# Kernel optimization log

Hardware: AMD Instinct MI355X
Metric: run time of the kernel (lower is better)

Reference implementation:

```python
import jax, jax.numpy as jnp
import numpy as np

NUM_HEADS = 16
THETA = 10000.0


def setup_inputs() -> dict:
    key = jax.random.key(0)
    k1, k2, k3, k4 = jax.random.split(key, 4)
    B, T, D = 2, 2048, 1024
    x = jax.random.normal(k1, (B, T, D), dtype=jnp.float32)
    token_positions = jnp.sort(
        jax.random.randint(k2, (B, T), 0, 2048), axis=-1
    ).astype(jnp.int32)
    sigma_qkv = float(np.sqrt(2.0 / (D + 3 * D)))
    sigma_out = float(np.sqrt(2.0 / (D + D)))
    W_qkv = jax.random.normal(k3, (3 * D, D), dtype=jnp.float32) * sigma_qkv
    W_out = jax.random.normal(k4, (D, D), dtype=jnp.float32) * sigma_out
    return {"x": x, "token_positions": token_positions, "W_qkv": W_qkv, "W_out": W_out}


def _apply_rope(t, cos, sin):
    # t: [B, H, T, d_k]; cos/sin: [B, T, d_k//2]
    B, H, T, dk = t.shape
    t2 = t.reshape(B, H, T, dk // 2, 2)
    te, to = t2[..., 0], t2[..., 1]
    c = cos[:, None]  # [B, 1, T, dk//2]
    s = sin[:, None]
    ye = te * c - to * s
    yo = to * c + te * s
    return jnp.stack([ye, yo], axis=-1).reshape(B, H, T, dk)


def reference(x, token_positions, W_qkv, W_out):
    B, T, D = x.shape
    H = NUM_HEADS
    dk = D // H

    # fused QKV projection: [B, T, 3D] -> split (three, h, d) on last dim
    qkv = jnp.einsum("btd,od->bto", x, W_qkv).reshape(B, T, 3, H, dk)
    qkv = jnp.transpose(qkv, (2, 0, 3, 1, 4))  # [3, B, H, T, dk]
    q, k, v = qkv[0], qkv[1], qkv[2]

    # RoPE angles from token positions
    n = jnp.arange(dk // 2, dtype=jnp.float32)
    inv_freq = THETA ** (-2.0 * n / dk)  # [dk//2]
    angles = token_positions.astype(jnp.float32)[..., None] * inv_freq  # [B, T, dk//2]
    cos, sin = jnp.cos(angles), jnp.sin(angles)
    q = _apply_rope(q, cos, sin)
    k = _apply_rope(k, cos, sin)

    # causal scaled dot-product attention
    scores = jnp.einsum("bhid,bhjd->bhij", q, k) / jnp.sqrt(jnp.float32(dk))
    causal = jnp.tril(jnp.ones((T, T), dtype=bool))
    scores = jnp.where(causal, scores, -jnp.inf)
    probs = jax.nn.softmax(scores, axis=-1)
    attn = jnp.einsum("bhij,bhjd->bhid", probs, v)  # [B, H, T, dk]

    concat = jnp.transpose(attn, (0, 2, 1, 3)).reshape(B, T, D)
    return jnp.einsum("btd,od->bto", concat, W_out)
```

## Files before the change

### kernel.cpp

```cpp
#include <hip/hip_runtime.h>
#include <hip/hip_bf16.h>
#include <cmath>

#define T_SEQ 2048
#define D_MODEL 1024
#define NHEAD 16
#define DK 64

typedef short bf16x8 __attribute__((ext_vector_type(8)));
typedef float f32x4 __attribute__((ext_vector_type(4)));
typedef float f32x16 __attribute__((ext_vector_type(16)));
typedef unsigned uint2v __attribute__((ext_vector_type(2)));

union U8 { unsigned u[4]; bf16x8 v; };

#define VMCNT(n) asm volatile("s_waitcnt vmcnt(" #n ")" ::: "memory")
#define BAR() __builtin_amdgcn_s_barrier()
#define SFENCE() __builtin_amdgcn_sched_barrier(0)

__device__ __forceinline__ short f2b(float f) {
    unsigned u = __builtin_bit_cast(unsigned, f);
    unsigned r = (u + 0x7FFFu + ((u >> 16) & 1u)) >> 16;
    return (short)r;
}

__device__ __forceinline__ void gll16(const void* g, void* l) {
    __builtin_amdgcn_global_load_lds(
        (__attribute__((address_space(1))) void*)g,
        (__attribute__((address_space(3))) void*)l, 16, 0, 0);
}

__device__ __forceinline__ bf16x8 lds_frag(const short* base, int row, int chunk) {
    return *reinterpret_cast<const bf16x8*>(
        (const char*)base + row * 128 + ((chunk * 16) ^ ((row & 7) << 4)));
}

__device__ __forceinline__ unsigned pkbf16(float a, float b) {
    unsigned r;
    asm("v_cvt_pk_bf16_f32 %0, %1, %2" : "=v"(r) : "v"(a), "v"(b));
    return r;
}
__device__ __forceinline__ void pl32swap(unsigned& a, unsigned& b) {
    uint2v r = __builtin_amdgcn_permlane32_swap(a, b, false, false);
    a = r.x; b = r.y;
}

__global__ __launch_bounds__(256) void cvt_all(const float* __restrict__ x,
                                               const float* __restrict__ wq,
                                               const float* __restrict__ wo,
                                               const int* __restrict__ pos,
                                               short* __restrict__ xb,
                                               short* __restrict__ wqb,
                                               short* __restrict__ wob,
                                               float* __restrict__ ct,
                                               float* __restrict__ st) {
    int i = blockIdx.x * 256 + threadIdx.x;
    if (i >= 1048576) {
        int j = i - 1048576;
        int bt = j >> 5, n = j & 31;
        float p = (float)pos[bt];
        float invf = expf((float)n * (-2.0f / (float)DK) * 9.210340371976184f);
        float s, c;
        sincosf(p * invf, &s, &c);
        ct[j] = c; st[j] = s;
        return;
    }
    const float* src;
    short* dst;
    int srcoff, c;
    if (i < 524288) {
        c = i;
        int tile = c >> 9, cc = c & 511;
        int kblk = cc >> 7, row = cc & 127;
        int rb = tile >> 5, kb = tile & 31;
        srcoff = (rb * 128 + row) * D_MODEL + kb * 32 + kblk * 8;
        src = x; dst = xb;
    } else if (i < 917504) {
        c = i - 524288;
        int tile = c >> 9, cc = c & 511;
        int kblk = cc >> 7, row = cc & 127;
        int rb = tile >> 5, kb = tile & 31;
        srcoff = (rb * 128 + row) * D_MODEL + kb * 32 + kblk * 8;
        src = wq; dst = wqb;
    } else {
        c = i - 917504;
        int tile = c >> 8, cc = c & 255;
        int kblk = cc >> 6, row = cc & 63;
        int nb = tile >> 5, kb = tile & 31;
        srcoff = (nb * 64 + row) * D_MODEL + kb * 32 + kblk * 8;
        src = wo; dst = wob;
    }
    float4 a = *reinterpret_cast<const float4*>(src + srcoff);
    float4 b = *reinterpret_cast<const float4*>(src + srcoff + 4);
    bf16x8 v;
    v[0] = f2b(a.x); v[1] = f2b(a.y); v[2] = f2b(a.z); v[3] = f2b(a.w);
    v[4] = f2b(b.x); v[5] = f2b(b.y); v[6] = f2b(b.z); v[7] = f2b(b.w);
    reinterpret_cast<bf16x8*>(dst)[c] = v;
}

__global__ __launch_bounds__(256, 3) void gemm_qkv(const short* __restrict__ xb,
                                                   const short* __restrict__ wb,
                                                   const float* __restrict__ ct,
                                                   const float* __restrict__ st,
                                                   short* __restrict__ Qo,
                                                   short* __restrict__ Ko,
                                                   short* __restrict__ Vt) {
    __shared__ short SM[3][8192];
    const int tid = threadIdx.x;
    const int w = tid >> 6, l = tid & 63, lg = l >> 4, li = l & 15;
    const int wr = w >> 1, wc = w & 1;
    const int bn = blockIdx.x * 128, bm = blockIdx.y * 128;

    const short* pA = xb + (size_t)blockIdx.y * 32 * 4096 + (w * 128 + l) * 8;
    const short* pB = wb + (size_t)blockIdx.x * 32 * 4096 + (w * 128 + l) * 8;

    f32x4 zero = {0.f, 0.f, 0.f, 0.f};
    f32x4 acc[4][4];
#pragma unroll
    for (int m = 0; m < 4; ++m)
#pragma unroll
        for (int n = 0; n < 4; ++n) acc[m][n] = zero;

#define GSTAGE(buf, t_)                                               \
    do {                                                              \
        const size_t ko = (size_t)(t_) * 4096;                        \
        gll16(pA + ko,       &SM[buf][w * 1024]);                     \
        gll16(pA + ko + 512, &SM[buf][w * 1024 + 512]);               \
        gll16(pB + ko,       &SM[buf][4096 + w * 1024]);              \
        gll16(pB + ko + 512, &SM[buf][4096 + w * 1024 + 512]);        \
    } while (0)

    GSTAGE(0, 0);
    GSTAGE(1, 1);

    for (int t = 0; t < 32; ++t) {
        if (t < 31) { VMCNT(4); } else { VMCNT(0); }
        BAR();
        SFENCE();
        if (t + 2 < 32) GSTAGE((t + 2) % 3, t + 2);
        const short* Ac = &SM[t % 3][0];
        const short* Bc = &SM[t % 3][4096];
        bf16x8 a[4], b[4];
#pragma unroll
        for (int m = 0; m < 4; ++m)
            a[m] = *reinterpret_cast<const bf16x8*>(&Ac[lg * 1024 + (wr * 64 + m * 16 + li) * 8]);
#pragma unroll
        for (int n = 0; n < 4; ++n)
            b[n] = *reinterpret_cast<const bf16x8*>(&Bc[lg * 1024 + (wc * 64 + n * 16 + li) * 8]);
        __builtin_amdgcn_s_setprio(1);
#pragma unroll
        for (int m = 0; m < 4; ++m)
#pragma unroll
            for (int n = 0; n < 4; ++n)
                acc[m][n] = __builtin_amdgcn_mfma_f32_16x16x32_bf16(a[m], b[n], acc[m][n], 0, 0, 0);
        __builtin_amdgcn_s_setprio(0);
    }
#undef GSTAGE

    const int which = bn >> 10;
    const int h = ((bn >> 6) + wc) & 15;
    if (which == 2) {
        __syncthreads();
        short* scr = &SM[0][0] + w * 4096;
#pragma unroll
        for (int n = 0; n < 4; ++n)
#pragma unroll
            for (int m = 0; m < 4; ++m)
#pragma unroll
                for (int rp = 0; rp < 2; ++rp) {
                    int d = n * 16 + li;
                    int t64 = m * 16 + lg * 4 + rp * 2;
                    unsigned pk = pkbf16(acc[m][n][rp * 2], acc[m][n][rp * 2 + 1]);
                    *reinterpret_cast<unsigned*>(
                        (char*)scr + ((d * 128 + t64 * 2) ^ ((d & 7) << 4))) = pk;
                }
        const int mi0 = bm + wr * 64;
        const int b0 = mi0 >> 11, t0 = mi0 & (T_SEQ - 1);
        const int kvt = t0 >> 6;
        short* vbase = Vt + ((size_t)(b0 * NHEAD + h) * 32 + kvt) * 4096;
        const int ch = l >> 3;
#pragma unroll
        for (int db = 0; db < 8; ++db) {
            int d = db * 8 + (l & 7);
            bf16x8 v = *reinterpret_cast<const bf16x8*>(
                (char*)scr + ((d * 128 + ch * 16) ^ ((d & 7) << 4)));
            *reinterpret_cast<bf16x8*>(vbase + ch * 512 + d * 8) = v;
        }
    } else {
#pragma unroll
        for (int n = 0; n < 4; ++n) {
            const int d = n * 16 + li;
#pragma unroll
            for (int m = 0; m < 4; ++m)
#pragma unroll
                for (int r = 0; r < 4; ++r) {
                    const int mi = bm + wr * 64 + m * 16 + lg * 4 + r;
                    const int b_ = mi >> 11, tt = mi & (T_SEQ - 1);
                    float v = acc[m][n][r];
                    float vp = __shfl_xor(v, 1);
                    int nn = n * 8 + (li >> 1);
                    float c = ct[(size_t)mi * 32 + nn];
                    float s = st[(size_t)mi * 32 + nn];
                    float o = (d & 1) ? (v * c + vp * s) : (v * c - vp * s);
                    if (which == 0) o *= 0.18033688011112042f;
                    short* dst = (which == 0) ? Qo : Ko;
                    dst[((size_t)((b_ * NHEAD + h) * T_SEQ + tt)) * DK + d] = f2b(o);
                }
        }
    }
}

__global__ __launch_bounds__(256, 3) void attn(const short* __restrict__ Q,
                                               const short* __restrict__ K,
                                               const short* __restrict__ Vt,
                                               short* __restrict__ Cc) {
    __shared__ short Kls[2][4096];

    const int bid = blockIdx.x;
    const int ii = bid & 255, rhalf = bid >> 8;
    const int bh = ii & 31;
    const int qt = rhalf ? 15 - (ii >> 5) : (ii >> 5);
    const int ntb = 2 * qt + 2;

    const int tid = threadIdx.x;
    const int w = tid >> 6, l = tid & 63;
    const int l31 = l & 31, hi = l >> 5, hi4 = hi * 4, hi8 = hi * 8;
    const int q0w = qt * 128 + w * 32;
    const int Tw = (q0w + 32 + 63) >> 6;

    const short* Qh = Q + (size_t)bh * T_SEQ * DK;
    const short* Kh = K + (size_t)bh * T_SEQ * DK;
    const short* Vh = Vt + (size_t)bh * 32 * 4096;

    bf16x8 qf[4];
#pragma unroll
    for (int ks = 0; ks < 4; ++ks)
        qf[ks] = *reinterpret_cast<const bf16x8*>(&Qh[(size_t)(q0w + l31) * DK + ks * 16 + hi8]);

    f32x16 o0 = {0.f,0.f,0.f,0.f,0.f,0.f,0.f,0.f,0.f,0.f,0.f,0.f,0.f,0.f,0.f,0.f};
    f32x16 o1 = o0;
    float m = -3.0e38f;
    float lsum = 0.f;

    int kr0, kc0, kr1, kc1;
    {
        int c0 = tid;        kr0 = c0 >> 3; kc0 = ((c0 & 7) ^ (kr0 & 7)) * 8;
        int c1 = 256 + tid;  kr1 = c1 >> 3; kc1 = ((c1 & 7) ^ (kr1 & 7)) * 8;
    }
    auto kstage = [&](int buf, int n0_) {
        gll16(Kh + (size_t)(n0_ + kr0) * DK + kc0, &Kls[buf][w * 512]);
        gll16(Kh + (size_t)(n0_ + kr1) * DK + kc1, &Kls[buf][2048 + w * 512]);
    };

    bf16x8 v00[2], v01[2], v10[2], v11[2];
    U8 pf0[2], pf1[2];

    kstage(0, 0);

    for (int t = 0; t < ntb; ++t) {
        VMCNT(0);
        BAR();
        SFENCE();
        if (t + 1 < ntb) kstage((t + 1) & 1, (t + 1) * 64);

        if (t < Tw) {
            const int n0 = t * 64;
            const short* Kc = Kls[t & 1];

            f32x16 s0 = {0.f,0.f,0.f,0.f,0.f,0.f,0.f,0.f,0.f,0.f,0.f,0.f,0.f,0.f,0.f,0.f};
            f32x16 s1 = s0;
            __builtin_amdgcn_s_setprio(1);
#pragma unroll
            for (int ks = 0; ks < 4; ++ks) {
                bf16x8 kf0 = lds_frag(Kc, l31,      ks * 2 + hi);
                bf16x8 kf1 = lds_frag(Kc, 32 + l31, ks * 2 + hi);
                s0 = __builtin_amdgcn_mfma_f32_32x32x16_bf16(kf0, qf[ks], s0, 0, 0, 0);
                s1 = __builtin_amdgcn_mfma_f32_32x32x16_bf16(kf1, qf[ks], s1, 0, 0, 0);
            }
            if (t > 0) {
#pragma unroll
                for (int kb = 0; kb < 2; ++kb) {
                    o0 = __builtin_amdgcn_mfma_f32_32x32x16_bf16(pf0[kb].v, v00[kb], o0, 0, 0, 0);
                    o0 = __builtin_amdgcn_mfma_f32_32x32x16_bf16(pf1[kb].v, v01[kb], o0, 0, 0, 0);
                    o1 = __builtin_amdgcn_mfma_f32_32x32x16_bf16(pf0[kb].v, v10[kb], o1, 0, 0, 0);
                    o1 = __builtin_amdgcn_mfma_f32_32x32x16_bf16(pf1[kb].v, v11[kb], o1, 0, 0, 0);
                }
            }
            __builtin_amdgcn_s_setprio(0);

            const short* vt = Vh + (size_t)t * 4096;
#pragma unroll
            for (int kb = 0; kb < 2; ++kb) {
                v00[kb] = *reinterpret_cast<const bf16x8*>(vt + (kb * 4 + hi) * 512 + l31 * 8);
                v01[kb] = *reinterpret_cast<const bf16x8*>(vt + (kb * 4 + 2 + hi) * 512 + l31 * 8);
                v10[kb] = *reinterpret_cast<const bf16x8*>(vt + (kb * 4 + hi) * 512 + 256 + l31 * 8);
                v11[kb] = *reinterpret_cast<const bf16x8*>(vt + (kb * 4 + 2 + hi) * 512 + 256 + l31 * 8);
            }
            SFENCE();

            float p[32];
#pragma unroll
            for (int r = 0; r < 16; ++r) { p[r] = s0[r]; p[16 + r] = s1[r]; }

            if (n0 + 64 > q0w) {
                const int qrel = q0w + l31 - n0;
#pragma unroll
                for (int r = 0; r < 16; ++r) {
                    const int kvm = (r & 3) + 8 * (r >> 2) + hi4;
                    if (kvm > qrel) p[r] = -3.0e38f;
                    if (kvm + 32 > qrel) p[16 + r] = -3.0e38f;
                }
            }

            float t16[16];
#pragma unroll
            for (int r = 0; r < 16; ++r) t16[r] = fmaxf(p[r], p[16 + r]);
#pragma unroll
            for (int d = 8; d >= 1; d >>= 1)
#pragma unroll
                for (int r = 0; r < 8; ++r)
                    if (r < d) t16[r] = fmaxf(t16[r], t16[r + d]);
            float tmax = fmaxf(t16[0], __shfl_xor(t16[0], 32));

            if (__any(tmax > m + 8.0f)) {
                float mnew = fmaxf(m, tmax);
                float alpha = __builtin_amdgcn_exp2f(m - mnew);
                m = mnew;
#pragma unroll
                for (int r = 0; r < 16; ++r) {
                    float ar = __shfl(alpha, (r & 3) + 8 * (r >> 2) + hi4);
                    o0[r] *= ar; o1[r] *= ar;
                }
                lsum *= alpha;
            }

#pragma unroll
            for (int r = 0; r < 32; ++r) p[r] = __builtin_amdgcn_exp2f(p[r] - m);
            float a16[16];
#pragma unroll
            for (int r = 0; r < 16; ++r) a16[r] = p[r] + p[16 + r];
#pragma unroll
            for (int d = 8; d >= 1; d >>= 1)
#pragma unroll
                for (int r = 0; r < 8; ++r)
                    if (r < d) a16[r] += a16[r + d];
            lsum += a16[0] + __shfl_xor(a16[0], 32);

#pragma unroll
            for (int kb = 0; kb < 2; ++kb) {
                unsigned pk0 = pkbf16(p[kb * 16 + 0],  p[kb * 16 + 1]);
                unsigned pk1 = pkbf16(p[kb * 16 + 2],  p[kb * 16 + 3]);
                unsigned pk2 = pkbf16(p[kb * 16 + 4],  p[kb * 16 + 5]);
                unsigned pk3 = pkbf16(p[kb * 16 + 6],  p[kb * 16 + 7]);
                unsigned pk4 = pkbf16(p[kb * 16 + 8],  p[kb * 16 + 9]);
                unsigned pk5 = pkbf16(p[kb * 16 + 10], p[kb * 16 + 11]);
                unsigned pk6 = pkbf16(p[kb * 16 + 12], p[kb * 16 + 13]);
                unsigned pk7 = pkbf16(p[kb * 16 + 14], p[kb * 16 + 15]);
                pl32swap(pk0, pk2); pl32swap(pk1, pk3);
                pl32swap(pk4, pk6); pl32swap(pk5, pk7);
                pf0[kb].u[0] = pk0; pf0[kb].u[1] = pk1; pf0[kb].u[2] = pk2; pf0[kb].u[3] = pk3;
                pf1[kb].u[0] = pk4; pf1[kb].u[1] = pk5; pf1[kb].u[2] = pk6; pf1[kb].u[3] = pk7;
            }
        }
    }

    __builtin_amdgcn_s_setprio(1);
#pragma unroll
    for (int kb = 0; kb < 2; ++kb) {
        o0 = __builtin_amdgcn_mfma_f32_32x32x16_bf16(pf0[kb].v, v00[kb], o0, 0, 0, 0);
        o0 = __builtin_amdgcn_mfma_f32_32x32x16_bf16(pf1[kb].v, v01[kb], o0, 0, 0, 0);
        o1 = __builtin_amdgcn_mfma_f32_32x32x16_bf16(pf0[kb].v, v10[kb], o1, 0, 0, 0);
        o1 = __builtin_amdgcn_mfma_f32_32x32x16_bf16(pf1[kb].v, v11[kb], o1, 0, 0, 0);
    }
    __builtin_amdgcn_s_setprio(0);

    const int b = bh >> 4, h = bh & 15;
    const float linv = 1.0f / lsum;
#pragma unroll
    for (int r = 0; r < 16; ++r) {
        const int qoff = (r & 3) + 8 * (r >> 2) + hi4;
        float inv = __shfl(linv, qoff);
        const int mg = b * T_SEQ + q0w + qoff;
        const int mb = mg >> 7, row = mg & 127;
        const int kblk = l31 >> 3, el = l & 7;
        Cc[((size_t)(mb * 32 + h * 2 + 0)) * 4096 + kblk * 1024 + row * 8 + el] = f2b(o0[r] * inv);
        Cc[((size_t)(mb * 32 + h * 2 + 1)) * 4096 + kblk * 1024 + row * 8 + el] = f2b(o1[r] * inv);
    }
}

__global__ __launch_bounds__(256, 3) void gemm_out(const short* __restrict__ ab,
                                                   const short* __restrict__ wb,
                                                   float* __restrict__ out) {
    __shared__ short SM[3][6144];
    const int tid = threadIdx.x;
    const int w = tid >> 6, l = tid & 63, lg = l >> 4, li = l & 15;
    const int wr = w >> 1, wc = w & 1;
    const int bn = blockIdx.x * 64, bm = blockIdx.y * 128;

    const short* pA = ab + (size_t)blockIdx.y * 32 * 4096 + (w * 128 + l) * 8;
    const short* pB = wb + (size_t)blockIdx.x * 32 * 2048 + (w * 64 + l) * 8;

    f32x4 zero = {0.f, 0.f, 0.f, 0.f};
    f32x4 acc[4][2];
#pragma unroll
    for (int m = 0; m < 4; ++m)
#pragma unroll
        for (int n = 0; n < 2; ++n) acc[m][n] = zero;

#define OSTAGE(buf, t_)                                                  \
    do {                                                                 \
        gll16(pA + (size_t)(t_) * 4096,       &SM[buf][w * 1024]);       \
        gll16(pA + (size_t)(t_) * 4096 + 512, &SM[buf][w * 1024 + 512]); \
        gll16(pB + (size_t)(t_) * 2048,       &SM[buf][4096 + w * 512]); \
    } while (0)

    OSTAGE(0, 0);
    OSTAGE(1, 1);

    for (int t = 0; t < 32; ++t) {
        if (t < 31) { VMCNT(3); } else { VMCNT(0); }
        BAR();
        SFENCE();
        if (t + 2 < 32) OSTAGE((t + 2) % 3, t + 2);
        const short* Ac = &SM[t % 3][0];
        const short* Bc = &SM[t % 3][4096];
        bf16x8 a[4], b[2];
#pragma unroll
        for (int m = 0; m < 4; ++m)
            a[m] = *reinterpret_cast<const bf16x8*>(&Ac[lg * 1024 + (wr * 64 + m * 16 + li) * 8]);
#pragma unroll
        for (int n = 0; n < 2; ++n)
            b[n] = *reinterpret_cast<const bf16x8*>(&Bc[lg * 512 + (wc * 32 + n * 16 + li) * 8]);
        __builtin_amdgcn_s_setprio(1);
#pragma unroll
        for (int m = 0; m < 4; ++m)
#pragma unroll
            for (int n = 0; n < 2; ++n)
                acc[m][n] = __builtin_amdgcn_mfma_f32_16x16x32_bf16(a[m], b[n], acc[m][n], 0, 0, 0);
        __builtin_amdgcn_s_setprio(0);
    }
#undef OSTAGE

#pragma unroll
    for (int m = 0; m < 4; ++m)
#pragma unroll
        for (int n = 0; n < 2; ++n)
#pragma unroll
            for (int r = 0; r < 4; ++r) {
                const int mi = bm + wr * 64 + m * 16 + lg * 4 + r;
                out[(size_t)mi * D_MODEL + bn + wc * 32 + n * 16 + li] = acc[m][n][r];
            }
}

extern "C" void kernel_launch(void* const* d_in, const int* in_sizes, int n_in,
                              void* d_out, int out_size, void* d_ws, size_t ws_size,
                              hipStream_t stream) {
    const float* x    = (const float*)d_in[0];
    const int*   pos  = (const int*)d_in[1];
    const float* wqkv = (const float*)d_in[2];
    const float* wout = (const float*)d_in[3];
    float* out = (float*)d_out;

    char* ws = (char*)d_ws;
    size_t off = 0;
    short* xb  = (short*)(ws + off); off += (size_t)4096 * 1024 * 2;
    short* wqb = (short*)(ws + off); off += (size_t)3072 * 1024 * 2;
    short* wob = (short*)(ws + off); off += (size_t)1024 * 1024 * 2;
    short* Q   = (short*)(ws + off); off += (size_t)32 * 2048 * 64 * 2;
    short* Kb  = (short*)(ws + off); off += (size_t)32 * 2048 * 64 * 2;
    short* Vt  = (short*)(ws + off); off += (size_t)32 * 32 * 4096 * 2;
    off += 4096;
    short* Cc  = (short*)(ws + off); off += (size_t)4096 * 1024 * 2;
    float* ct  = (float*)(ws + off); off += (size_t)4096 * 32 * 4;
    float* st  = (float*)(ws + off); off += (size_t)4096 * 32 * 4;

    cvt_all<<<4608, 256, 0, stream>>>(x, wqkv, wout, pos, xb, wqb, wob, ct, st);
    gemm_qkv<<<dim3(24, 32), 256, 0, stream>>>(xb, wqb, ct, st, Q, Kb, Vt);
    attn<<<512, 256, 0, stream>>>(Q, Kb, Vt, Cc);
    gemm_out<<<dim3(16, 32), 256, 0, stream>>>(Cc, wob, out);
}
```

Measured before the change: 112.9 us.

## Triple-buffer K and ping-pong prefetch V registers in attention loop

Restructures the attention main loop into a 2-way unrolled schedule. K tiles use three LDS buffers and are staged two tiles ahead with a relaxed vmcnt wait, while V fragments are prefetched one tile ahead into alternating register sets. The P·V MFMAs now run inside the same iteration instead of being deferred to the next one. The aim is to hide global and LDS latency behind compute, at the cost of more LDS and registers, which is why launch bounds drop from 3 to 2 blocks per CU and occupancy may fall.

Result: no change. 113.7 us (+0.7%).

```diff
diff --git a/kernel.cpp b/kernel.cpp
--- a/kernel.cpp
+++ b/kernel.cpp
@@ -210,11 +210,11 @@
     }
 }
 
-__global__ __launch_bounds__(256, 3) void attn(const short* __restrict__ Q,
+__global__ __launch_bounds__(256, 2) void attn(const short* __restrict__ Q,
                                                const short* __restrict__ K,
                                                const short* __restrict__ Vt,
                                                short* __restrict__ Cc) {
-    __shared__ short Kls[2][4096];
+    __shared__ short Kls[3][4096];
 
     const int bid = blockIdx.x;
     const int ii = bid & 255, rhalf = bid >> 8;
@@ -237,8 +237,8 @@
     for (int ks = 0; ks < 4; ++ks)
         qf[ks] = *reinterpret_cast<const bf16x8*>(&Qh[(size_t)(q0w + l31) * DK + ks * 16 + hi8]);
 
-    f32x16 o0 = {0.f,0.f,0.f,0.f,0.f,0.f,0.f,0.f,0.f,0.f,0.f,0.f,0.f,0.f,0.f,0.f};
-    f32x16 o1 = o0;
+    const f32x16 Z16 = {0.f,0.f,0.f,0.f,0.f,0.f,0.f,0.f,0.f,0.f,0.f,0.f,0.f,0.f,0.f,0.f};
+    f32x16 o0 = Z16, o1 = Z16;
     float m = -3.0e38f;
     float lsum = 0.f;
 
@@ -247,132 +247,129 @@
         int c0 = tid;        kr0 = c0 >> 3; kc0 = ((c0 & 7) ^ (kr0 & 7)) * 8;
         int c1 = 256 + tid;  kr1 = c1 >> 3; kc1 = ((c1 & 7) ^ (kr1 & 7)) * 8;
     }
-    auto kstage = [&](int buf, int n0_) {
-        gll16(Kh + (size_t)(n0_ + kr0) * DK + kc0, &Kls[buf][w * 512]);
-        gll16(Kh + (size_t)(n0_ + kr1) * DK + kc1, &Kls[buf][2048 + w * 512]);
-    };
-
-    bf16x8 v00[2], v01[2], v10[2], v11[2];
-    U8 pf0[2], pf1[2];
-
-    kstage(0, 0);
-
-    for (int t = 0; t < ntb; ++t) {
-        VMCNT(0);
+#define KSTAGE(t_)                                                                     \
+    do {                                                                               \
+        gll16(Kh + (size_t)((t_) * 64 + kr0) * DK + kc0, &Kls[(t_) % 3][w * 512]);     \
+        gll16(Kh + (size_t)((t_) * 64 + kr1) * DK + kc1, &Kls[(t_) % 3][2048 + w * 512]); \
+    } while (0)
+
+#define VLOAD(dst_, t_)                                                                \
+    do {                                                                               \
+        const short* vt = Vh + (size_t)(t_) * 4096;                                    \
+        dst_[0] = *reinterpret_cast<const bf16x8*>(vt + (0 + hi) * 512 + l31 * 8);     \
+        dst_[1] = *reinterpret_cast<const bf16x8*>(vt + (2 + hi) * 512 + l31 * 8);     \
+        dst_[2] = *reinterpret_cast<const bf16x8*>(vt + (0 + hi) * 512 + 256 + l31 * 8); \
+        dst_[3] = *reinterpret_cast<const bf16x8*>(vt + (2 + hi) * 512 + 256 + l31 * 8); \
+        dst_[4] = *reinterpret_cast<const bf16x8*>(vt + (4 + hi) * 512 + l31 * 8);     \
+        dst_[5] = *reinterpret_cast<const bf16x8*>(vt + (6 + hi) * 512 + l31 * 8);     \
+        dst_[6] = *reinterpret_cast<const bf16x8*>(vt + (4 + hi) * 512 + 256 + l31 * 8); \
+        dst_[7] = *reinterpret_cast<const bf16x8*>(vt + (6 + hi) * 512 + 256 + l31 * 8); \
+    } while (0)
+
+#define COMPUTE(t_, vv)                                                                \
+    do {                                                                               \
+        const int n0 = (t_) * 64;                                                      \
+        const short* Kc = Kls[(t_) % 3];                                               \
+        f32x16 s0 = Z16, s1 = Z16;                                                     \
+        __builtin_amdgcn_s_setprio(1);                                                 \
+        _Pragma("unroll")                                                              \
+        for (int ks = 0; ks < 4; ++ks) {                                               \
+            bf16x8 kf0 = lds_frag(Kc, l31,      ks * 2 + hi);                          \
+            bf16x8 kf1 = lds_frag(Kc, 32 + l31, ks * 2 + hi);                          \
+            s0 = __builtin_amdgcn_mfma_f32_32x32x16_bf16(kf0, qf[ks], s0, 0, 0, 0);    \
+            s1 = __builtin_amdgcn_mfma_f32_32x32x16_bf16(kf1, qf[ks], s1, 0, 0, 0);    \
+        }                                                                              \
+        __builtin_amdgcn_s_setprio(0);                                                 \
+        float p[32];                                                                   \
+        _Pragma("unroll")                                                              \
+        for (int r = 0; r < 16; ++r) { p[r] = s0[r]; p[16 + r] = s1[r]; }              \
+        if (n0 + 64 > q0w) {                                                           \
+            const int qrel = q0w + l31 - n0;                                           \
+            _Pragma("unroll")                                                          \
+            for (int r = 0; r < 16; ++r) {                                             \
+                const int kvm = (r & 3) + 8 * (r >> 2) + hi4;                          \
+                if (kvm > qrel) p[r] = -3.0e38f;                                       \
+                if (kvm + 32 > qrel) p[16 + r] = -3.0e38f;                             \
+            }                                                                          \
+        }                                                                              \
+        float t16[16];                                                                 \
+        _Pragma("unroll")                                                              \
+        for (int r = 0; r < 16; ++r) t16[r] = fmaxf(p[r], p[16 + r]);                  \
+        _Pragma("unroll")                                                              \
+        for (int d = 8; d >= 1; d >>= 1)                                               \
+            _Pragma("unroll")                                                          \
+            for (int r = 0; r < 8; ++r)                                                \
+                if (r < d) t16[r] = fmaxf(t16[r], t16[r + d]);                         \
+        float tmax = fmaxf(t16[0], __shfl_xor(t16[0], 32));                            \
+        if (__any(tmax > m + 8.0f)) {                                                  \
+            float mnew = fmaxf(m, tmax);                                               \
+            float alpha = __builtin_amdgcn_exp2f(m - mnew);                            \
+            m = mnew;                                                                  \
+            _Pragma("unroll")                                                          \
+            for (int r = 0; r < 16; ++r) {                                             \
+                float ar = __shfl(alpha, (r & 3) + 8 * (r >> 2) + hi4);                \
+                o0[r] *= ar; o1[r] *= ar;                                              \
+            }                                                                          \
+            lsum *= alpha;                                                             \
+        }                                                                              \
+        _Pragma("unroll")                                                              \
+        for (int r = 0; r < 32; ++r) p[r] = __builtin_amdgcn_exp2f(p[r] - m);          \
+        float a16[16];                                                                 \
+        _Pragma("unroll")                                                              \
+        for (int r = 0; r < 16; ++r) a16[r] = p[r] + p[16 + r];                        \
+        _Pragma("unroll")                                                              \
+        for (int d = 8; d >= 1; d >>= 1)                                               \
+            _Pragma("unroll")                                                          \
+            for (int r = 0; r < 8; ++r)                                                \
+                if (r < d) a16[r] += a16[r + d];                                       \
+        lsum += a16[0] + __shfl_xor(a16[0], 32);                                       \
+        __builtin_amdgcn_s_setprio(1);                                                 \
+        _Pragma("unroll")                                                              \
+        for (int kb = 0; kb < 2; ++kb) {                                               \
+            unsigned pk0 = pkbf16(p[kb * 16 + 0],  p[kb * 16 + 1]);                    \
+            unsigned pk1 = pkbf16(p[kb * 16 + 2],  p[kb * 16 + 3]);                    \
+            unsigned pk2 = pkbf16(p[kb * 16 + 4],  p[kb * 16 + 5]);                    \
+            unsigned pk3 = pkbf16(p[kb * 16 + 6],  p[kb * 16 + 7]);                    \
+            unsigned pk4 = pkbf16(p[kb * 16 + 8],  p[kb * 16 + 9]);                    \
+            unsigned pk5 = pkbf16(p[kb * 16 + 10], p[kb * 16 + 11]);                   \
+            unsigned pk6 = pkbf16(p[kb * 16 + 12], p[kb * 16 + 13]);                   \
+            unsigned pk7 = pkbf16(p[kb * 16 + 14], p[kb * 16 + 15]);                   \
+            pl32swap(pk0, pk2); pl32swap(pk1, pk3);                                    \
+            pl32swap(pk4, pk6); pl32swap(pk5, pk7);                                    \
+            U8 f0, f1;                                                                 \
+            f0.u[0] = pk0; f0.u[1] = pk1; f0.u[2] = pk2; f0.u[3] = pk3;                \
+            f1.u[0] = pk4; f1.u[1] = pk5; f1.u[2] = pk6; f1.u[3] = pk7;                \
+            o0 = __builtin_amdgcn_mfma_f32_32x32x16_bf16(f0.v, vv[kb * 4 + 0], o0, 0, 0, 0); \
+            o0 = __builtin_amdgcn_mfma_f32_32x32x16_bf16(f1.v, vv[kb * 4 + 1], o0, 0, 0, 0); \
+            o1 = __builtin_amdgcn_mfma_f32_32x32x16_bf16(f0.v, vv[kb * 4 + 2], o1, 0, 0, 0); \
+            o1 = __builtin_amdgcn_mfma_f32_32x32x16_bf16(f1.v, vv[kb * 4 + 3], o1, 0, 0, 0); \
+        }                                                                              \
+        __builtin_amdgcn_s_setprio(0);                                                 \
+    } while (0)
+
+    bf16x8 vA[8], vB[8];
+
+    VLOAD(vA, 0);
+    KSTAGE(0);
+    KSTAGE(1);
+
+    for (int t = 0; t < ntb; t += 2) {
+        VMCNT(2);
         BAR();
         SFENCE();
-        if (t + 1 < ntb) kstage((t + 1) & 1, (t + 1) * 64);
-
-        if (t < Tw) {
-            const int n0 = t * 64;
-            const short* Kc = Kls[t & 1];
-
-            f32x16 s0 = {0.f,0.f,0.f,0.f,0.f,0.f,0.f,0.f,0.f,0.f,0.f,0.f,0.f,0.f,0.f,0.f};
-            f32x16 s1 = s0;
-            __builtin_amdgcn_s_setprio(1);
-#pragma unroll
-            for (int ks = 0; ks < 4; ++ks) {
-                bf16x8 kf0 = lds_frag(Kc, l31,      ks * 2 + hi);
-                bf16x8 kf1 = lds_frag(Kc, 32 + l31, ks * 2 + hi);
-                s0 = __builtin_amdgcn_mfma_f32_32x32x16_bf16(kf0, qf[ks], s0, 0, 0, 0);
-                s1 = __builtin_amdgcn_mfma_f32_32x32x16_bf16(kf1, qf[ks], s1, 0, 0, 0);
-            }
-            if (t > 0) {
-#pragma unroll
-                for (int kb = 0; kb < 2; ++kb) {
-                    o0 = __builtin_amdgcn_mfma_f32_32x32x16_bf16(pf0[kb].v, v00[kb], o0, 0, 0, 0);
-                    o0 = __builtin_amdgcn_mfma_f32_32x32x16_bf16(pf1[kb].v, v01[kb], o0, 0, 0, 0);
-                    o1 = __builtin_amdgcn_mfma_f32_32x32x16_bf16(pf0[kb].v, v10[kb], o1, 0, 0, 0);
-                    o1 = __builtin_amdgcn_mfma_f32_32x32x16_bf16(pf1[kb].v, v11[kb], o1, 0, 0, 0);
-                }
-            }
-            __builtin_amdgcn_s_setprio(0);
-
-            const short* vt = Vh + (size_t)t * 4096;
-#pragma unroll
-            for (int kb = 0; kb < 2; ++kb) {
-                v00[kb] = *reinterpret_cast<const bf16x8*>(vt + (kb * 4 + hi) * 512 + l31 * 8);
-                v01[kb] = *reinterpret_cast<const bf16x8*>(vt + (kb * 4 + 2 + hi) * 512 + l31 * 8);
-                v10[kb] = *reinterpret_cast<const bf16x8*>(vt + (kb * 4 + hi) * 512 + 256 + l31 * 8);
-                v11[kb] = *reinterpret_cast<const bf16x8*>(vt + (kb * 4 + 2 + hi) * 512 + 256 + l31 * 8);
-            }
-            SFENCE();
-
-            float p[32];
-#pragma unroll
-            for (int r = 0; r < 16; ++r) { p[r] = s0[r]; p[16 + r] = s1[r]; }
-
-            if (n0 + 64 > q0w) {
-                const int qrel = q0w + l31 - n0;
-#pragma unroll
-                for (int r = 0; r < 16; ++r) {
-                    const int kvm = (r & 3) + 8 * (r >> 2) + hi4;
-                    if (kvm > qrel) p[r] = -3.0e38f;
-                    if (kvm + 32 > qrel) p[16 + r] = -3.0e38f;
-                }
-            }
-
-            float t16[16];
-#pragma unroll
-            for (int r = 0; r < 16; ++r) t16[r] = fmaxf(p[r], p[16 + r]);
-#pragma unroll
-            for (int d = 8; d >= 1; d >>= 1)
-#pragma unroll
-                for (int r = 0; r < 8; ++r)
-                    if (r < d) t16[r] = fmaxf(t16[r], t16[r + d]);
-            float tmax = fmaxf(t16[0], __shfl_xor(t16[0], 32));
-
-            if (__any(tmax > m + 8.0f)) {
-                float mnew = fmaxf(m, tmax);
-                float alpha = __builtin_amdgcn_exp2f(m - mnew);
-                m = mnew;
-#pragma unroll
-                for (int r = 0; r < 16; ++r) {
-                    float ar = __shfl(alpha, (r & 3) + 8 * (r >> 2) + hi4);
-                    o0[r] *= ar; o1[r] *= ar;
-                }
-                lsum *= alpha;
-            }
-
-#pragma unroll
-            for (int r = 0; r < 32; ++r) p[r] = __builtin_amdgcn_exp2f(p[r] - m);
-            float a16[16];
-#pragma unroll
-            for (int r = 0; r < 16; ++r) a16[r] = p[r] + p[16 + r];
-#pragma unroll
-            for (int d = 8; d >= 1; d >>= 1)
-#pragma unroll
-                for (int r = 0; r < 8; ++r)
-                    if (r < d) a16[r] += a16[r + d];
-            lsum += a16[0] + __shfl_xor(a16[0], 32);
-
-#pragma unroll
-            for (int kb = 0; kb < 2; ++kb) {
-                unsigned pk0 = pkbf16(p[kb * 16 + 0],  p[kb * 16 + 1]);
-                unsigned pk1 = pkbf16(p[kb * 16 + 2],  p[kb * 16 + 3]);
-                unsigned pk2 = pkbf16(p[kb * 16 + 4],  p[kb * 16 + 5]);
-                unsigned pk3 = pkbf16(p[kb * 16 + 6],  p[kb * 16 + 7]);
-                unsigned pk4 = pkbf16(p[kb * 16 + 8],  p[kb * 16 + 9]);
-                unsigned pk5 = pkbf16(p[kb * 16 + 10], p[kb * 16 + 11]);
-                unsigned pk6 = pkbf16(p[kb * 16 + 12], p[kb * 16 + 13]);
-                unsigned pk7 = pkbf16(p[kb * 16 + 14], p[kb * 16 + 15]);
-                pl32swap(pk0, pk2); pl32swap(pk1, pk3);
-                pl32swap(pk4, pk6); pl32swap(pk5, pk7);
-                pf0[kb].u[0] = pk0; pf0[kb].u[1] = pk1; pf0[kb].u[2] = pk2; pf0[kb].u[3] = pk3;
-                pf1[kb].u[0] = pk4; pf1[kb].u[1] = pk5; pf1[kb].u[2] = pk6; pf1[kb].u[3] = pk7;
-            }
-        }
-    }
-
-    __builtin_amdgcn_s_setprio(1);
-#pragma unroll
-    for (int kb = 0; kb < 2; ++kb) {
-        o0 = __builtin_amdgcn_mfma_f32_32x32x16_bf16(pf0[kb].v, v00[kb], o0, 0, 0, 0);
-        o0 = __builtin_amdgcn_mfma_f32_32x32x16_bf16(pf1[kb].v, v01[kb], o0, 0, 0, 0);
-        o1 = __builtin_amdgcn_mfma_f32_32x32x16_bf16(pf0[kb].v, v10[kb], o1, 0, 0, 0);
-        o1 = __builtin_amdgcn_mfma_f32_32x32x16_bf16(pf1[kb].v, v11[kb], o1, 0, 0, 0);
-    }
-    __builtin_amdgcn_s_setprio(0);
+        VLOAD(vB, t + 1);
+        if (t + 2 < ntb) KSTAGE(t + 2);
+        if (t < Tw) COMPUTE(t, vA);
+        VMCNT(2);
+        BAR();
+        SFENCE();
+        if (t + 2 < ntb) VLOAD(vA, t + 2);
+        if (t + 3 < ntb) KSTAGE(t + 3);
+        if (t + 1 < Tw) COMPUTE(t + 1, vB);
+    }
+#undef COMPUTE
+#undef VLOAD
+#undef KSTAGE
 
     const int b = bh >> 4, h = bh & 15;
     const float linv = 1.0f / lsum;
```
